# Performance work log

Hardware: AMD Instinct MI355X
Metric: run time of the kernel (lower is better)

Reference implementation:

```python
import jax, jax.numpy as jnp
import numpy as np


def setup_inputs() -> dict:
    key = jax.random.key(0)
    k1, k2 = jax.random.split(key)
    B, C, L, K = 32, 64, 4096, 512
    inputs = jax.random.normal(k1, (B, C, L), dtype=jnp.float32)
    # codebook init: uniform(-1/K, 1/K) as in the torch module
    embed = jax.random.uniform(k2, (K, C), dtype=jnp.float32, minval=-1.0 / K, maxval=1.0 / K)
    return {"inputs": inputs, "embed": embed}


def reference(inputs, embed):
    commitment_cost = 0.25
    b, c, l = inputs.shape
    K = embed.shape[0]
    # (B, C, L) -> (B*L, C)
    flat = jnp.transpose(inputs, (0, 2, 1)).reshape(-1, c)
    flat_sq = jnp.sum(flat * flat, axis=1, keepdims=True)            # (N, 1)
    embed_sq = jnp.sum(embed * embed, axis=1)                        # (K,)
    distances = flat_sq + embed_sq[None, :] - 2.0 * (flat @ embed.T)  # (N, K)
    encoding_indices = jnp.argmin(distances, axis=1)                 # (N,)
    encodings = jax.nn.one_hot(encoding_indices, K, dtype=flat.dtype)  # (N, K)
    # gather codewords (equivalent to one_hot @ embed) and restore (B, C, L)
    quantized = jnp.transpose(embed[encoding_indices].reshape(b, l, c), (0, 2, 1))
    e_latent_loss = jnp.mean((jax.lax.stop_gradient(quantized) - inputs) ** 2)
    q_latent_loss = jnp.mean((quantized - jax.lax.stop_gradient(inputs)) ** 2)
    loss = q_latent_loss + commitment_cost * e_latent_loss
    # straight-through estimator
    quantized_st = inputs + jax.lax.stop_gradient(quantized - inputs)
    avg_probs = jnp.mean(encodings, axis=0)                          # (K,)
    perplexity = jnp.exp(-jnp.sum(avg_probs * jnp.log(avg_probs + 1e-10)))
    return (loss, quantized_st, perplexity, embed, encoding_indices.reshape(b, l), encodings)
```

## Files before the change

kernel.cpp:

```cpp
#include <hip/hip_runtime.h>
#include <math.h>

#define B_DIM 32
#define C_DIM 64
#define L_DIM 4096
#define K_CB  512
#define N_ROWS (B_DIM * L_DIM)
#define Q_ELEMS (B_DIM * C_DIM * L_DIM)

#define OFF_LOSS  0
#define OFF_Q     1
#define OFF_PERP  (1 + Q_ELEMS)
#define OFF_EMBED (OFF_PERP + 1)
#define OFF_IDX   (OFF_EMBED + K_CB * C_DIM)
#define OFF_ENC   (OFF_IDX + N_ROWS)

#define TPB     128
#define RPB     256
#define KCHUNK  128

using f4 = __attribute__((ext_vector_type(4))) float;
using f2 = __attribute__((ext_vector_type(2))) float;


__global__ void vq_init(const float* __restrict__ embed,
                        double* __restrict__ loss_ws,
                        int* __restrict__ hist,
                        float* __restrict__ esq,
                        float* __restrict__ out_embed) {
  const int t = threadIdx.x;
  if (t == 0) *loss_ws = 0.0;
  hist[t] = 0;
  const float* row = embed + (size_t)t * C_DIM;
  float s = 0.f;
#pragma unroll
  for (int c = 0; c < C_DIM; ++c) s = fmaf(row[c], row[c], s);
  esq[t] = s;
#pragma unroll
  for (int i = 0; i < K_CB * C_DIM / 512; ++i)
    out_embed[i * 512 + t] = embed[i * 512 + t];
}

__global__ __launch_bounds__(TPB) void vq_fused(
    const float* __restrict__ in, const float* __restrict__ embed,
    const float* __restrict__ esq_g, int* __restrict__ hist,
    double* __restrict__ loss_ws, float* __restrict__ out) {
  __shared__ float  eT[KCHUNK * C_DIM];
  __shared__ float  esq_s[KCHUNK];
  __shared__ double red[TPB];

  const int tid = threadIdx.x;
  const int blk = blockIdx.x;
  const int b   = blk >> 4;
  const int l0  = (blk & 15) * RPB;
  const int l   = l0 + 2 * tid;

  const float* xp = in + (size_t)b * (C_DIM * L_DIM) + l;
  f2 x[C_DIM];
#pragma unroll
  for (int c = 0; c < C_DIM; ++c) x[c] = *(const f2*)(xp + (size_t)c * L_DIM);

  float fs0 = 0.f, fs1 = 0.f;
#pragma unroll
  for (int c = 0; c < C_DIM; ++c) {
    fs0 = fmaf(x[c].x, x[c].x, fs0);
    fs1 = fmaf(x[c].y, x[c].y, fs1);
  }

  f2* encz = (f2*)(out + OFF_ENC) + (size_t)blk * RPB * (K_CB / 2);
  f2 zz; zz.x = 0.f; zz.y = 0.f;

  float rmin0 = 3.402823466e38f, rmin1 = 3.402823466e38f;
  int   ridx0 = 0, ridx1 = 0;

  for (int kc = 0; kc < K_CB / KCHUNK; ++kc) {
    const int k0 = kc * KCHUNK;
    __syncthreads();
#pragma unroll
    for (int i = 0; i < 16; ++i) {
      const int o = i * 512 + tid * 4;
      *(f4*)&eT[o] = *(const f4*)(embed + (size_t)k0 * C_DIM + o);
    }
    esq_s[tid] = esq_g[k0 + tid];
    __syncthreads();

    for (int kk = 0; kk < KCHUNK; kk += 8) {
      float a0[8], a1[8];
#pragma unroll
      for (int j = 0; j < 8; ++j) { a0[j] = 0.f; a1[j] = 0.f; }
#pragma unroll
      for (int cq = 0; cq < 16; ++cq) {
        f4 ev[8];
#pragma unroll
        for (int j = 0; j < 8; ++j)
          ev[j] = *(const f4*)&eT[(kk + j) * C_DIM + cq * 4];
#pragma unroll
        for (int q = 0; q < 4; ++q) {
          const f2 xv = x[cq * 4 + q];
#pragma unroll
          for (int j = 0; j < 8; ++j) {
            a0[j] = fmaf(xv.x, ev[j][q], a0[j]);
            a1[j] = fmaf(xv.y, ev[j][q], a1[j]);
          }
        }
      }
      {
        const int g = (k0 + kk) >> 3;
#pragma unroll
        for (int s = 0; s < 8; ++s)
          __builtin_nontemporal_store(zz, encz + (size_t)(g * 8 + s) * TPB + tid);
      }
#pragma unroll
      for (int j = 0; j < 8; ++j) {
        const int k = k0 + kk + j;
        const float es = esq_s[kk + j];
        const float d0 = fmaf(-2.0f, a0[j], fs0 + es);
        if (d0 < rmin0) { rmin0 = d0; ridx0 = k; }
        const float d1 = fmaf(-2.0f, a1[j], fs1 + es);
        if (d1 < rmin1) { rmin1 = d1; ridx1 = k; }
      }
    }
  }

  {
    f2 iv; iv.x = (float)ridx0; iv.y = (float)ridx1;
    *(f2*)&out[OFF_IDX + blk * RPB + 2 * tid] = iv;
    atomicAdd(&hist[ridx0], 1);
    atomicAdd(&hist[ridx1], 1);
  }

  asm volatile("s_waitcnt vmcnt(0)" ::: "memory");
  __syncthreads();
  {
    float* encb = out + OFF_ENC + (size_t)blk * RPB * K_CB;
    encb[(size_t)(2 * tid) * K_CB + ridx0]     = 1.0f;
    encb[(size_t)(2 * tid + 1) * K_CB + ridx1] = 1.0f;
  }

  double ls = 0.0;
  {
    float* qbase = out + OFF_Q + (size_t)b * (C_DIM * L_DIM) + l;
    const float* e0 = embed + (size_t)ridx0 * C_DIM;
    const float* e1 = embed + (size_t)ridx1 * C_DIM;
#pragma unroll
    for (int c = 0; c < C_DIM; ++c) {
      const float q0 = e0[c], q1 = e1[c];
      const float d0 = q0 - x[c].x;
      const float d1 = q1 - x[c].y;
      __builtin_nontemporal_store(x[c].x + d0, qbase + (size_t)c * L_DIM);
      __builtin_nontemporal_store(x[c].y + d1, qbase + (size_t)c * L_DIM + 1);
      ls += (double)(d0 * d0);
      ls += (double)(d1 * d1);
    }
  }

  red[tid] = ls;
  __syncthreads();
  for (int s = 64; s; s >>= 1) {
    if (tid < s) red[tid] += red[tid + s];
    __syncthreads();
  }
  if (tid == 0) atomicAdd(loss_ws, red[0]);
}

__global__ void vq_final(const int* __restrict__ hist, const double* __restrict__ loss_ws,
                         float* __restrict__ out) {
  __shared__ float red[512];
  const int t = threadIdx.x;
  const float p = (float)hist[t] * (1.0f / (float)N_ROWS);
  red[t] = p * logf(p + 1e-10f);
  __syncthreads();
  for (int s = 256; s; s >>= 1) {
    if (t < s) red[t] += red[t + s];
    __syncthreads();
  }
  if (t == 0) {
    out[OFF_PERP] = expf(-red[0]);
    const float m = (float)(*loss_ws / (double)Q_ELEMS);
    out[OFF_LOSS] = m + 0.25f * m;
  }
}

extern "C" void kernel_launch(void* const* d_in, const int* in_sizes, int n_in,
                              void* d_out, int out_size, void* d_ws, size_t ws_size,
                              hipStream_t stream) {
  (void)in_sizes; (void)n_in; (void)out_size; (void)ws_size;
  const float* in    = (const float*)d_in[0];
  const float* embed = (const float*)d_in[1];
  float* out = (float*)d_out;

  double* loss_ws = (double*)d_ws;
  int*    hist    = (int*)((char*)d_ws + 16);
  float*  esq     = (float*)((char*)d_ws + 4096);

  vq_init<<<1, 512, 0, stream>>>(embed, loss_ws, hist, esq, out + OFF_EMBED);
  vq_fused<<<N_ROWS / RPB, TPB, 0, stream>>>(in, embed, esq, hist, loss_ws, out);
  vq_final<<<1, 512, 0, stream>>>(hist, loss_ws, out);
}
```

Measured before the change: 209.1 us.

## Keep codewords in registers and stream input rows via LDS with wave argmin

The distance kernel is restructured so that each thread holds two codewords in registers and the block's 128 input rows are transposed into padded LDS. For each row, every thread computes two dot products, and the argmin is found with cross-lane shuffles and a ballot, then merged across the four waves through shared memory. This removes the per-chunk reloads of the codebook into LDS and the many LDS vector reads per FMA. In exchange it adds a wave reduction per row, strided global loads for the transpose, and 128 registers of codeword data per thread, which may limit occupancy.

```diff
diff --git a/kernel.cpp b/kernel.cpp
--- a/kernel.cpp
+++ b/kernel.cpp
@@ -15,9 +15,9 @@
 #define OFF_IDX   (OFF_EMBED + K_CB * C_DIM)
 #define OFF_ENC   (OFF_IDX + N_ROWS)
 
-#define TPB     128
-#define RPB     256
-#define KCHUNK  128
+#define TPB 256
+#define TM  128
+#define XPAD 68
 
 using f4 = __attribute__((ext_vector_type(4))) float;
 using f2 = __attribute__((ext_vector_type(2))) float;
@@ -45,118 +45,121 @@
     const float* __restrict__ in, const float* __restrict__ embed,
     const float* __restrict__ esq_g, int* __restrict__ hist,
     double* __restrict__ loss_ws, float* __restrict__ out) {
-  __shared__ float  eT[KCHUNK * C_DIM];
-  __shared__ float  esq_s[KCHUNK];
+  __shared__ __align__(16) float xT[TM][XPAD];
+  __shared__ float  fs_s[TM];
+  __shared__ f2     part[TM][4];
+  __shared__ int    k_s[TM];
   __shared__ double red[TPB];
 
   const int tid = threadIdx.x;
   const int blk = blockIdx.x;
-  const int b   = blk >> 4;
-  const int l0  = (blk & 15) * RPB;
-  const int l   = l0 + 2 * tid;
-
-  const float* xp = in + (size_t)b * (C_DIM * L_DIM) + l;
-  f2 x[C_DIM];
-#pragma unroll
-  for (int c = 0; c < C_DIM; ++c) x[c] = *(const f2*)(xp + (size_t)c * L_DIM);
-
-  float fs0 = 0.f, fs1 = 0.f;
-#pragma unroll
-  for (int c = 0; c < C_DIM; ++c) {
-    fs0 = fmaf(x[c].x, x[c].x, fs0);
-    fs1 = fmaf(x[c].y, x[c].y, fs1);
-  }
-
-  f2* encz = (f2*)(out + OFF_ENC) + (size_t)blk * RPB * (K_CB / 2);
+  const int R0  = blk * TM;
+  const int b   = blk >> 5;
+  const int l0  = (blk & 31) * TM;
+
+  {
+    const float* xb = in + (size_t)b * (C_DIM * L_DIM) + l0;
+#pragma unroll
+    for (int i = 0; i < 32; ++i) {
+      const int flat = i * TPB + tid;
+      const int r = flat & (TM - 1);
+      const int c = flat >> 7;
+      xT[r][c] = xb[(size_t)c * L_DIM + r];
+    }
+  }
+
+  const int cw0 = 2 * tid, cw1 = 2 * tid + 1;
+  f4 e0[16], e1[16];
+#pragma unroll
+  for (int q = 0; q < 16; ++q) {
+    e0[q] = *(const f4*)(embed + (size_t)cw0 * C_DIM + 4 * q);
+    e1[q] = *(const f4*)(embed + (size_t)cw1 * C_DIM + 4 * q);
+  }
+  const float esq0 = esq_g[cw0];
+  const float esq1 = esq_g[cw1];
+
+  __syncthreads();
+
+  if (tid < TM) {
+    float s = 0.f;
+#pragma unroll
+    for (int c = 0; c < C_DIM; ++c) { const float v = xT[tid][c]; s = fmaf(v, v, s); }
+    fs_s[tid] = s;
+  }
+  __syncthreads();
+
+  const int wv = tid >> 6;
+  const int ln = tid & 63;
+  f2* encb = (f2*)(out + OFF_ENC) + (size_t)R0 * (K_CB / 2);
   f2 zz; zz.x = 0.f; zz.y = 0.f;
 
-  float rmin0 = 3.402823466e38f, rmin1 = 3.402823466e38f;
-  int   ridx0 = 0, ridx1 = 0;
-
-  for (int kc = 0; kc < K_CB / KCHUNK; ++kc) {
-    const int k0 = kc * KCHUNK;
-    __syncthreads();
-#pragma unroll
-    for (int i = 0; i < 16; ++i) {
-      const int o = i * 512 + tid * 4;
-      *(f4*)&eT[o] = *(const f4*)(embed + (size_t)k0 * C_DIM + o);
-    }
-    esq_s[tid] = esq_g[k0 + tid];
-    __syncthreads();
-
-    for (int kk = 0; kk < KCHUNK; kk += 8) {
-      float a0[8], a1[8];
-#pragma unroll
-      for (int j = 0; j < 8; ++j) { a0[j] = 0.f; a1[j] = 0.f; }
-#pragma unroll
-      for (int cq = 0; cq < 16; ++cq) {
-        f4 ev[8];
-#pragma unroll
-        for (int j = 0; j < 8; ++j)
-          ev[j] = *(const f4*)&eT[(kk + j) * C_DIM + cq * 4];
-#pragma unroll
-        for (int q = 0; q < 4; ++q) {
-          const f2 xv = x[cq * 4 + q];
-#pragma unroll
-          for (int j = 0; j < 8; ++j) {
-            a0[j] = fmaf(xv.x, ev[j][q], a0[j]);
-            a1[j] = fmaf(xv.y, ev[j][q], a1[j]);
-          }
-        }
+  for (int r = 0; r < TM; ++r) {
+    const f4* xr = (const f4*)&xT[r][0];
+    float a0 = 0.f, a1 = 0.f;
+#pragma unroll
+    for (int q = 0; q < 16; ++q) {
+      const f4 xq = xr[q];
+#pragma unroll
+      for (int i = 0; i < 4; ++i) {
+        a0 = fmaf(xq[i], e0[q][i], a0);
+        a1 = fmaf(xq[i], e1[q][i], a1);
       }
-      {
-        const int g = (k0 + kk) >> 3;
-#pragma unroll
-        for (int s = 0; s < 8; ++s)
-          __builtin_nontemporal_store(zz, encz + (size_t)(g * 8 + s) * TPB + tid);
-      }
-#pragma unroll
-      for (int j = 0; j < 8; ++j) {
-        const int k = k0 + kk + j;
-        const float es = esq_s[kk + j];
-        const float d0 = fmaf(-2.0f, a0[j], fs0 + es);
-        if (d0 < rmin0) { rmin0 = d0; ridx0 = k; }
-        const float d1 = fmaf(-2.0f, a1[j], fs1 + es);
-        if (d1 < rmin1) { rmin1 = d1; ridx1 = k; }
-      }
-    }
-  }
-
-  {
-    f2 iv; iv.x = (float)ridx0; iv.y = (float)ridx1;
-    *(f2*)&out[OFF_IDX + blk * RPB + 2 * tid] = iv;
-    atomicAdd(&hist[ridx0], 1);
-    atomicAdd(&hist[ridx1], 1);
+    }
+    const float fsr = fs_s[r];
+    const float d0 = fmaf(-2.0f, a0, fsr + esq0);
+    const float d1 = fmaf(-2.0f, a1, fsr + esq1);
+    float md; int mk;
+    if (d1 < d0) { md = d1; mk = cw1; } else { md = d0; mk = cw0; }
+
+    float dm = md;
+#pragma unroll
+    for (int off = 32; off; off >>= 1) dm = fminf(dm, __shfl_xor(dm, off));
+    const unsigned long long m = __ballot(md == dm);
+    const int src = __ffsll(m) - 1;
+    const int kk  = __shfl(mk, src);
+    if (ln == 0) { f2 p; p.x = dm; p.y = (float)kk; part[r][wv] = p; }
+
+    __builtin_nontemporal_store(zz, encb + (size_t)r * (K_CB / 2) + tid);
+  }
+  __syncthreads();
+
+  if (tid < TM) {
+    f2 p = part[tid][0];
+    float bd = p.x; int bk = (int)p.y;
+#pragma unroll
+    for (int w = 1; w < 4; ++w) {
+      const f2 q = part[tid][w];
+      if (q.x < bd) { bd = q.x; bk = (int)q.y; }
+    }
+    k_s[tid] = bk;
+    out[OFF_IDX + R0 + tid] = (float)bk;
+    atomicAdd(&hist[bk], 1);
   }
 
   asm volatile("s_waitcnt vmcnt(0)" ::: "memory");
   __syncthreads();
-  {
-    float* encb = out + OFF_ENC + (size_t)blk * RPB * K_CB;
-    encb[(size_t)(2 * tid) * K_CB + ridx0]     = 1.0f;
-    encb[(size_t)(2 * tid + 1) * K_CB + ridx1] = 1.0f;
-  }
+  if (tid < TM)
+    out[OFF_ENC + (size_t)(R0 + tid) * K_CB + k_s[tid]] = 1.0f;
 
   double ls = 0.0;
   {
-    float* qbase = out + OFF_Q + (size_t)b * (C_DIM * L_DIM) + l;
-    const float* e0 = embed + (size_t)ridx0 * C_DIM;
-    const float* e1 = embed + (size_t)ridx1 * C_DIM;
-#pragma unroll
-    for (int c = 0; c < C_DIM; ++c) {
-      const float q0 = e0[c], q1 = e1[c];
-      const float d0 = q0 - x[c].x;
-      const float d1 = q1 - x[c].y;
-      __builtin_nontemporal_store(x[c].x + d0, qbase + (size_t)c * L_DIM);
-      __builtin_nontemporal_store(x[c].y + d1, qbase + (size_t)c * L_DIM + 1);
-      ls += (double)(d0 * d0);
-      ls += (double)(d1 * d1);
+    float* qb = out + OFF_Q + (size_t)b * (C_DIM * L_DIM) + l0;
+#pragma unroll 4
+    for (int it = 0; it < 32; ++it) {
+      const int flat = it * TPB + tid;
+      const int r = flat & (TM - 1);
+      const int c = flat >> 7;
+      const float x = xT[r][c];
+      const float q = embed[(size_t)k_s[r] * C_DIM + c];
+      const float d = q - x;
+      __builtin_nontemporal_store(x + d, qb + (size_t)c * L_DIM + r);
+      ls += (double)(d * d);
     }
   }
 
   red[tid] = ls;
   __syncthreads();
-  for (int s = 64; s; s >>= 1) {
+  for (int s = 128; s; s >>= 1) {
     if (tid < s) red[tid] += red[tid + s];
     __syncthreads();
   }
@@ -194,6 +197,6 @@
   float*  esq     = (float*)((char*)d_ws + 4096);
 
   vq_init<<<1, 512, 0, stream>>>(embed, loss_ws, hist, esq, out + OFF_EMBED);
-  vq_fused<<<N_ROWS / RPB, TPB, 0, stream>>>(in, embed, esq, hist, loss_ws, out);
+  vq_fused<<<N_ROWS / TM, TPB, 0, stream>>>(in, embed, esq, hist, loss_ws, out);
   vq_final<<<1, 512, 0, stream>>>(hist, loss_ws, out);
 }
```

Result: slower. 243.0 us (+16.2%).
